# Kernel optimization log

Hardware: AMD Instinct MI355X
Metric: run time of the kernel (lower is better)

Reference implementation:

```python
import jax, jax.numpy as jnp
import numpy as np

N = 10000        # nodes
E = 120000       # edges
IN_W = 6         # in_width
KER_IN = 6       # edge-attr dim
WN = 32          # width_node
WK = 256         # width_kernel
DEPTH = 4


def setup_inputs() -> dict:
    key = jax.random.key(0)
    ks = jax.random.split(key, 16)

    def w(k, shape, fan_in):
        return (jax.random.normal(k, shape, jnp.float32) / np.sqrt(fan_in)).astype(jnp.float32)

    return {
        "x": jax.random.normal(ks[0], (N, IN_W), jnp.float32),
        "edge_index": jax.random.randint(ks[1], (2, E), 0, N, jnp.int64 if jax.config.jax_enable_x64 else jnp.int32),
        "edge_attr": jax.random.uniform(ks[2], (E, KER_IN), jnp.float32),
        # fc1: in_width -> width_node
        "fc1_w": w(ks[3], (IN_W, WN), IN_W), "fc1_b": jnp.zeros((WN,), jnp.float32),
        # DenseNet kernel: ker_in -> WK//2 -> WK -> WN*WN (ReLU between, none after last)
        "k1_w": w(ks[4], (KER_IN, WK // 2), KER_IN), "k1_b": jnp.zeros((WK // 2,), jnp.float32),
        "k2_w": w(ks[5], (WK // 2, WK), WK // 2),    "k2_b": jnp.zeros((WK,), jnp.float32),
        "k3_w": w(ks[6], (WK, WN * WN), WK),         "k3_b": jnp.zeros((WN * WN,), jnp.float32),
        # NNConv root weight + bias
        "root_w": w(ks[7], (WN, WN), WN), "conv_b": jnp.zeros((WN,), jnp.float32),
        # fc2: WN -> 128, fc3: 128 -> 1
        "fc2_w": w(ks[8], (WN, 128), WN), "fc2_b": jnp.zeros((128,), jnp.float32),
        "fc3_w": w(ks[9], (128, 1), 128), "fc3_b": jnp.zeros((1,), jnp.float32),
    }


def reference(x, edge_index, edge_attr,
              fc1_w, fc1_b, k1_w, k1_b, k2_w, k2_b, k3_w, k3_b,
              root_w, conv_b, fc2_w, fc2_b, fc3_w, fc3_b):
    src, dst = edge_index[0], edge_index[1]

    # Edge-conditioned weight matrices via DenseNet kernel MLP (same edge_attr
    # every layer -> identical weights each depth step; compute once).
    h_e = jax.nn.relu(edge_attr @ k1_w + k1_b)
    h_e = jax.nn.relu(h_e @ k2_w + k2_b)
    w_e = (h_e @ k3_w + k3_b).reshape(E, WN, WN)   # [E, in, out]

    # scatter-mean denominator (in-degree, clamped to 1)
    cnt = jax.ops.segment_sum(jnp.ones((E,), jnp.float32), dst, num_segments=N)
    denom = jnp.maximum(cnt, 1.0)[:, None]

    h = x @ fc1_w + fc1_b                          # [N, WN]
    for d in range(DEPTH):
        msg = jnp.einsum('ei,eio->eo', h[src], w_e)          # per-edge matvec
        aggr = jax.ops.segment_sum(msg, dst, num_segments=N) / denom
        h = aggr + h @ root_w + conv_b             # NNConv: aggr + root + bias
        if d != DEPTH - 1:
            h = jax.nn.relu(h)

    h = jax.nn.relu(h @ fc2_w + fc2_b)
    return h @ fc3_w + fc3_b                       # [N, 1]
```

## Files before the change

kernel.cpp:

```cpp
#include <hip/hip_runtime.h>
#include <hip/hip_bf16.h>

#define NN 10000
#define EE 120000
#define E_PAD 120064
#define NT64 1876

#define H1S 136
#define H2S 264

typedef __bf16 bf16_t;
typedef __bf16 bf16x8 __attribute__((ext_vector_type(8)));
typedef float f32x4 __attribute__((ext_vector_type(4)));

static __device__ __forceinline__ int clampi(int v) {
    return v < 0 ? 0 : (v >= NN ? NN - 1 : v);
}

__global__ __launch_bounds__(256) void detect_all(const unsigned short* __restrict__ ea_raw,
                                                  const int* __restrict__ ei,
                                                  int* __restrict__ f32fl,
                                                  int* __restrict__ idxfl) {
    int t = blockIdx.x * 256 + threadIdx.x;
    if (ea_raw[t] & 0x8000) atomicOr(f32fl, 1);
    if (t < 4096 && ei[2 * t + 1] != 0) atomicOr(idxfl, 1);
}

#define N_FLT 16
struct CvtArgs {
    const void* src[N_FLT];
    float* dst;
    int offs[N_FLT];
    int n[N_FLT];
    int tot;
};

__global__ __launch_bounds__(256) void cvt_flat(CvtArgs a, const int* __restrict__ isf32) {
    int i = blockIdx.x * 256 + threadIdx.x;
    if (i >= a.tot) return;
    int t = 0;
#pragma unroll
    for (int k = 1; k < N_FLT; ++k) if (i >= a.offs[k]) t = k;
    int il = i - a.offs[t];
    float v;
    if (*isf32) v = ((const float*)a.src[t])[il];
    else        v = (float)((const bf16_t*)a.src[t])[il];
    if (!isfinite(v)) v = 0.f;
    a.dst[i] = v;
}

__global__ __launch_bounds__(256) void repack_idx(const int* __restrict__ ei,
                                                  const int* __restrict__ flag,
                                                  int* __restrict__ s,
                                                  int* __restrict__ d,
                                                  int* __restrict__ cnti) {
    int e = blockIdx.x * 256 + threadIdx.x;
    if (e >= EE) return;
    int sv, dv;
    if (*flag == 0) {
        sv = clampi(ei[2 * e]);
        dv = clampi(ei[2 * (EE + e)]);
    } else {
        sv = clampi(ei[e]);
        dv = clampi(ei[EE + e]);
    }
    s[e] = sv;
    d[e] = dv;
    atomicAdd(&cnti[dv], 1);
}

__global__ __launch_bounds__(256) void scan_kernel(const int* __restrict__ cnti,
                                                   int* __restrict__ row_off,
                                                   int* __restrict__ pos) {
    __shared__ int part[256];
    const int t = threadIdx.x;
    const int CH = (NN + 255) / 256;
    int s = 0;
    for (int i = 0; i < CH; ++i) {
        int idx = t * CH + i;
        if (idx < NN) s += cnti[idx];
    }
    part[t] = s;
    __syncthreads();
    for (int off = 1; off < 256; off <<= 1) {
        int tmp = (t >= off) ? part[t - off] : 0;
        __syncthreads();
        part[t] += tmp;
        __syncthreads();
    }
    int run = part[t] - s;
    for (int i = 0; i < CH; ++i) {
        int idx = t * CH + i;
        if (idx < NN) {
            row_off[idx] = run;
            pos[idx] = run;
            run += cnti[idx];
        }
    }
    if (t == 255) row_off[NN] = run;
}

__global__ __launch_bounds__(256) void scatter_rank(const int* __restrict__ dst,
                                                    const int* __restrict__ src,
                                                    int* __restrict__ pos,
                                                    int* __restrict__ rank,
                                                    int* __restrict__ src_s) {
    int e = blockIdx.x * 256 + threadIdx.x;
    if (e >= E_PAD) return;
    if (e >= EE) { rank[e] = e; return; }
    int p = atomicAdd(&pos[dst[e]], 1);
    rank[e] = p;
    src_s[p] = src[e];
}

__global__ __launch_bounds__(256) void misc_prep(const float* __restrict__ k2w,
                                                 bf16_t* __restrict__ k2t,
                                                 const float* __restrict__ k3w,
                                                 bf16_t* __restrict__ k3t,
                                                 const float* __restrict__ k3b,
                                                 float* __restrict__ k3bp,
                                                 const float* __restrict__ x,
                                                 const float* __restrict__ fc1w,
                                                 const float* __restrict__ fc1b,
                                                 float* __restrict__ h0) {
    int i = blockIdx.x * 256 + threadIdx.x;
    if (i < 32768) {
        int n = i >> 7, k = i & 127;
        k2t[i] = (bf16_t)k2w[k * 256 + n];
    } else if (i < 294912) {
        int idx = i - 32768;
        int n = idx >> 8, k = idx & 255;
        int c = ((n & 31) << 5) | (n >> 5);
        k3t[idx] = (bf16_t)k3w[k * 1024 + c];
    } else if (i < 295936) {
        int n = i - 294912;
        k3bp[n] = k3b[((n & 31) << 5) | (n >> 5)];
    } else if (i < 615936) {
        int gid = i - 295936;
        int n = gid >> 5, o = gid & 31;
        float acc = fc1b[o];
#pragma unroll
        for (int j = 0; j < 6; ++j) acc += x[n * 6 + j] * fc1w[j * 32 + o];
        h0[gid] = acc;
    }
}

__global__ __launch_bounds__(256, 3) void fused_prep(const float* __restrict__ ea,
                                                     const float* __restrict__ k1w,
                                                     const float* __restrict__ k1b,
                                                     const bf16_t* __restrict__ k2t,
                                                     const float* __restrict__ k2b,
                                                     const bf16_t* __restrict__ k3t,
                                                     const float* __restrict__ k3bp,
                                                     bf16_t* __restrict__ we,
                                                     const int* __restrict__ rank,
                                                     int tile0, int perm) {
    __shared__ bf16_t h1_s[64 * H1S];
    __shared__ bf16_t h2_s[64 * H2S];
    float* ea_s  = (float*)h2_s;
    float* k1w_s = ea_s + 64 * 6;
    float* k1b_s = k1w_s + 768;

    const int t = threadIdx.x;
    const int tile = tile0 + blockIdx.x;
    const int e0 = tile * 64;

    for (int i = t; i < 384; i += 256) {
        int r = i / 6, j = i - r * 6;
        int e = e0 + r;
        ea_s[i] = (e < EE) ? ea[(size_t)e * 6 + j] : 0.f;
    }
    for (int i = t; i < 768; i += 256) k1w_s[i] = k1w[i];
    if (t < 128) k1b_s[t] = k1b[t];
    __syncthreads();

    {
        const int o = t & 127, rh = t >> 7;
        for (int r = rh * 32; r < rh * 32 + 32; ++r) {
            float acc = k1b_s[o];
#pragma unroll
            for (int j = 0; j < 6; ++j) acc += ea_s[r * 6 + j] * k1w_s[j * 128 + o];
            h1_s[r * H1S + o] = (bf16_t)fmaxf(acc, 0.f);
        }
    }
    __syncthreads();

    const int lane = t & 63;
    const int w = t >> 6;
    const int nr16 = lane & 15;
    const int koff = (lane >> 4) * 8;
    const int rbase = (lane >> 4) * 4;

    {
        f32x4 acc[4][4];
#pragma unroll
        for (int i = 0; i < 4; ++i)
#pragma unroll
            for (int j = 0; j < 4; ++j) acc[i][j] = f32x4{0.f, 0.f, 0.f, 0.f};
        bf16x8 bcur[4], bnxt[4];
#pragma unroll
        for (int j = 0; j < 4; ++j)
            bcur[j] = *(const bf16x8*)&k2t[(w * 64 + j * 16 + nr16) * 128 + koff];
#pragma unroll 1
        for (int ks = 0; ks < 4; ++ks) {
            const int k0 = ks * 32;
            if (ks < 3) {
#pragma unroll
                for (int j = 0; j < 4; ++j)
                    bnxt[j] = *(const bf16x8*)&k2t[(w * 64 + j * 16 + nr16) * 128 + k0 + 32 + koff];
            }
            bf16x8 af[4];
#pragma unroll
            for (int i = 0; i < 4; ++i)
                af[i] = *(const bf16x8*)&h1_s[(nr16 + i * 16) * H1S + k0 + koff];
#pragma unroll
            for (int i = 0; i < 4; ++i)
#pragma unroll
                for (int j = 0; j < 4; ++j)
                    acc[i][j] = __builtin_amdgcn_mfma_f32_16x16x32_bf16(af[i], bcur[j], acc[i][j], 0, 0, 0);
#pragma unroll
            for (int j = 0; j < 4; ++j) bcur[j] = bnxt[j];
        }
#pragma unroll
        for (int i = 0; i < 4; ++i) {
#pragma unroll
            for (int j = 0; j < 4; ++j) {
                int col = w * 64 + j * 16 + nr16;
                float bv = k2b[col];
#pragma unroll
                for (int r = 0; r < 4; ++r) {
                    int row = i * 16 + rbase + r;
                    h2_s[row * H2S + col] = (bf16_t)fmaxf(acc[i][j][r] + bv, 0.f);
                }
            }
        }
    }
    __syncthreads();

    int crow[4][4];
#pragma unroll
    for (int i = 0; i < 4; ++i)
#pragma unroll
        for (int r = 0; r < 4; ++r) {
            int lr = i * 16 + rbase + r;
            crow[i][r] = perm ? rank[e0 + lr] : (int)blockIdx.x * 64 + lr;
        }

#pragma unroll 1
    for (int nt = 0; nt < 4; ++nt) {
        const int c0 = nt * 256 + w * 64;
        float bj[4];
#pragma unroll
        for (int j = 0; j < 4; ++j) bj[j] = k3bp[c0 + j * 16 + nr16];
        f32x4 acc[4][4];
#pragma unroll
        for (int i = 0; i < 4; ++i)
#pragma unroll
            for (int j = 0; j < 4; ++j) acc[i][j] = f32x4{0.f, 0.f, 0.f, 0.f};
        bf16x8 bcur[4], bnxt[4];
#pragma unroll
        for (int j = 0; j < 4; ++j)
            bcur[j] = *(const bf16x8*)&k3t[(size_t)(c0 + j * 16 + nr16) * 256 + koff];
#pragma unroll 1
        for (int ks = 0; ks < 8; ++ks) {
            const int k0 = ks * 32;
            if (ks < 7) {
#pragma unroll
                for (int j = 0; j < 4; ++j)
                    bnxt[j] = *(const bf16x8*)&k3t[(size_t)(c0 + j * 16 + nr16) * 256 + k0 + 32 + koff];
            }
            bf16x8 af[4];
#pragma unroll
            for (int i = 0; i < 4; ++i)
                af[i] = *(const bf16x8*)&h2_s[(nr16 + i * 16) * H2S + k0 + koff];
#pragma unroll
            for (int i = 0; i < 4; ++i)
#pragma unroll
                for (int j = 0; j < 4; ++j)
                    acc[i][j] = __builtin_amdgcn_mfma_f32_16x16x32_bf16(af[i], bcur[j], acc[i][j], 0, 0, 0);
#pragma unroll
            for (int j = 0; j < 4; ++j) bcur[j] = bnxt[j];
        }
#pragma unroll
        for (int i = 0; i < 4; ++i) {
#pragma unroll
            for (int r = 0; r < 4; ++r) {
                long cr = crow[i][r];
#pragma unroll
                for (int j = 0; j < 4; ++j) {
                    int col = c0 + j * 16 + nr16;
                    we[cr * 1024 + col] = (bf16_t)(acc[i][j][r] + bj[j]);
                }
            }
        }
    }
}

__global__ __launch_bounds__(256) void gather_stream(const float* __restrict__ h,
                                                     const bf16_t* __restrict__ wt,
                                                     const int* __restrict__ src_s,
                                                     const int* __restrict__ row_off,
                                                     const float* __restrict__ rw,
                                                     const float* __restrict__ cb,
                                                     float* __restrict__ hout,
                                                     int relu, int rev) {
    __shared__ float rws[1024];
    for (int i = threadIdx.x; i < 1024; i += 256) rws[i] = rw[i];
    __syncthreads();
    const int wv = threadIdx.x >> 6, lane = threadIdx.x & 63;
    const int nb = rev ? ((int)gridDim.x - 1 - blockIdx.x) : blockIdx.x;
    const int n = nb * 4 + wv;
    if (n >= NN) return;
    const int o = lane >> 1, half = lane & 1;

    const int b0 = row_off[n], b1 = row_off[n + 1];
    float acc = 0.f;
    if (b0 < b1) {
        int s = src_s[b0];
        const float4* hp = (const float4*)(h + (size_t)s * 32 + half * 16);
        float4 ha = hp[0], hb = hp[1], hcv = hp[2], hd = hp[3];
        const bf16x8* wp = (const bf16x8*)(wt + (size_t)b0 * 1024 + lane * 16);
        bf16x8 w0 = wp[0], w1 = wp[1];
        for (int k = b0; k + 1 < b1; ++k) {
            int s2 = src_s[k + 1];
            const float4* hp2 = (const float4*)(h + (size_t)s2 * 32 + half * 16);
            float4 na = hp2[0], nb2 = hp2[1], nc = hp2[2], nd = hp2[3];
            const bf16x8* wp2 = (const bf16x8*)(wt + (size_t)(k + 1) * 1024 + lane * 16);
            bf16x8 nw0 = wp2[0], nw1 = wp2[1];
            acc += ha.x * (float)w0[0] + ha.y * (float)w0[1]
                 + ha.z * (float)w0[2] + ha.w * (float)w0[3]
                 + hb.x * (float)w0[4] + hb.y * (float)w0[5]
                 + hb.z * (float)w0[6] + hb.w * (float)w0[7]
                 + hcv.x * (float)w1[0] + hcv.y * (float)w1[1]
                 + hcv.z * (float)w1[2] + hcv.w * (float)w1[3]
                 + hd.x * (float)w1[4] + hd.y * (float)w1[5]
                 + hd.z * (float)w1[6] + hd.w * (float)w1[7];
            ha = na; hb = nb2; hcv = nc; hd = nd; w0 = nw0; w1 = nw1;
        }
        acc += ha.x * (float)w0[0] + ha.y * (float)w0[1]
             + ha.z * (float)w0[2] + ha.w * (float)w0[3]
             + hb.x * (float)w0[4] + hb.y * (float)w0[5]
             + hb.z * (float)w0[6] + hb.w * (float)w0[7]
             + hcv.x * (float)w1[0] + hcv.y * (float)w1[1]
             + hcv.z * (float)w1[2] + hcv.w * (float)w1[3]
             + hd.x * (float)w1[4] + hd.y * (float)w1[5]
             + hd.z * (float)w1[6] + hd.w * (float)w1[7];
    }

    float rp = 0.f;
    const float4* hn = (const float4*)(h + (size_t)n * 32 + half * 16);
    float4 a = hn[0], b = hn[1], c = hn[2], dd = hn[3];
    const float* rwb = &rws[half * 16 * 32 + o];
    rp += a.x * rwb[0]   + a.y * rwb[32]  + a.z * rwb[64]  + a.w * rwb[96];
    rp += b.x * rwb[128] + b.y * rwb[160] + b.z * rwb[192] + b.w * rwb[224];
    rp += c.x * rwb[256] + c.y * rwb[288] + c.z * rwb[320] + c.w * rwb[352];
    rp += dd.x * rwb[384] + dd.y * rwb[416] + dd.z * rwb[448] + dd.w * rwb[480];

    acc += __shfl_xor(acc, 1, 64);
    rp  += __shfl_xor(rp, 1, 64);
    if (half == 0) {
        float den = fmaxf((float)(b1 - b0), 1.f);
        float v = acc / den + rp + cb[o];
        if (relu) v = fmaxf(v, 0.f);
        hout[(size_t)n * 32 + o] = v;
    }
}

__global__ __launch_bounds__(256) void edge_scatter(const float* __restrict__ h,
                                                    const bf16_t* __restrict__ wt,
                                                    const int* __restrict__ src,
                                                    const int* __restrict__ dst,
                                                    float* __restrict__ aggr,
                                                    int e0, int e1) {
    int wv = threadIdx.x >> 6, lane = threadIdx.x & 63;
    int e = e0 + blockIdx.x * 4 + wv;
    if (e >= e1) return;
    int s = src[e], d = dst[e];
    int o = lane & 31, ihalf = lane >> 5;
    const float4* hp = (const float4*)(h + (size_t)s * 32 + ihalf * 16);
    float4 ha = hp[0], hb = hp[1], hcv = hp[2], hd = hp[3];
    const bf16x8* wp = (const bf16x8*)(wt + (size_t)(e - e0) * 1024 + o * 32 + ihalf * 16);
    bf16x8 w0 = wp[0], w1 = wp[1];
    float acc = ha.x * (float)w0[0] + ha.y * (float)w0[1]
              + ha.z * (float)w0[2] + ha.w * (float)w0[3]
              + hb.x * (float)w0[4] + hb.y * (float)w0[5]
              + hb.z * (float)w0[6] + hb.w * (float)w0[7]
              + hcv.x * (float)w1[0] + hcv.y * (float)w1[1]
              + hcv.z * (float)w1[2] + hcv.w * (float)w1[3]
              + hd.x * (float)w1[4] + hd.y * (float)w1[5]
              + hd.z * (float)w1[6] + hd.w * (float)w1[7];
    acc += __shfl_xor(acc, 32, 64);
    if (ihalf == 0) atomicAdd(&aggr[(size_t)d * 32 + o], acc);
}

__global__ __launch_bounds__(256) void node_update(const float* __restrict__ hin,
                                                   const float* __restrict__ aggr,
                                                   const int* __restrict__ cnti,
                                                   const float* __restrict__ rw,
                                                   const float* __restrict__ cb,
                                                   float* __restrict__ hout, int relu) {
    __shared__ float rws[32 * 32];
    for (int i = threadIdx.x; i < 1024; i += 256) rws[i] = rw[i];
    __syncthreads();
    int gid = blockIdx.x * 256 + threadIdx.x;
    int n = gid >> 5, o = gid & 31;
    float den = fmaxf((float)cnti[n], 1.f);
    float acc = aggr[gid] / den + cb[o];
    const float* hrow = hin + (size_t)n * 32;
#pragma unroll
    for (int j = 0; j < 32; ++j) acc += hrow[j] * rws[j * 32 + o];
    if (relu) acc = fmaxf(acc, 0.f);
    hout[gid] = acc;
}

__global__ __launch_bounds__(256) void head_kernel(const float* __restrict__ h,
                                                   const float* __restrict__ w2,
                                                   const float* __restrict__ b2,
                                                   const float* __restrict__ w3,
                                                   const float* __restrict__ b3,
                                                   void* __restrict__ out,
                                                   const int* __restrict__ isf32) {
    int wave = threadIdx.x >> 6, lane = threadIdx.x & 63;
    int n = blockIdx.x * 4 + wave;
    if (n >= NN) return;
    const float* hrow = h + (size_t)n * 32;
    float hr[32];
#pragma unroll
    for (int j = 0; j < 32; ++j) hr[j] = hrow[j];
    int o0 = lane * 2, o1 = lane * 2 + 1;
    float v0 = b2[o0], v1 = b2[o1];
#pragma unroll
    for (int j = 0; j < 32; ++j) {
        float hj = hr[j];
        v0 += hj * w2[j * 128 + o0];
        v1 += hj * w2[j * 128 + o1];
    }
    float y = fmaxf(v0, 0.f) * w3[o0] + fmaxf(v1, 0.f) * w3[o1];
#pragma unroll
    for (int m = 1; m < 64; m <<= 1) y += __shfl_xor(y, m, 64);
    if (lane == 0) {
        float r = y + b3[0];
        if (*isf32) ((float*)out)[n] = r;
        else        ((bf16_t*)out)[n] = (bf16_t)r;
    }
}


extern "C" void kernel_launch(void* const* d_in, const int* in_sizes, int n_in,
                              void* d_out, int out_size, void* d_ws, size_t ws_size,
                              hipStream_t stream) {
    const int* ei = (const int*)d_in[1];

    char* ws = (char*)d_ws;
    size_t off = 0;
    auto alignup = [](size_t b) { return (b + 255) & ~(size_t)255; };
    auto alloc = [&](size_t bytes) {
        char* p = ws + off;
        off += alignup(bytes);
        return (void*)p;
    };
    float*  h_a   = (float*)alloc((size_t)NN * 32 * 4);
    float*  h_b   = (float*)alloc((size_t)NN * 32 * 4);
    char*   zbase = ws + off;
    int*    cnti  = (int*)alloc((size_t)NN * 4);
    int*    f32fl = (int*)alloc(256);
    int*    idxfl = (int*)alloc(256);
    size_t  zlen  = (ws + off) - zbase;
    int*    rowo  = (int*)alloc((size_t)(NN + 1) * 4);
    int*    pos   = (int*)alloc((size_t)NN * 4);
    int*    srcb  = (int*)alloc((size_t)EE * 4);
    int*    dstb  = (int*)alloc((size_t)EE * 4);
    int*    rankb = (int*)alloc((size_t)E_PAD * 4);
    int*    src_s = (int*)alloc((size_t)E_PAD * 4);
    bf16_t* k2t   = (bf16_t*)alloc(256 * 128 * 2);
    bf16_t* k3t   = (bf16_t*)alloc(1024 * 256 * 2);
    float*  k3bp  = (float*)alloc(1024 * 4);

    static const int fidx[N_FLT] = {0, 2, 3, 4, 5, 6, 7, 8, 9, 10, 11, 12, 13, 14, 15, 16};
    static const int fn[N_FLT]   = {NN * 6, EE * 6, 192, 32, 768, 128, 32768, 256,
                                    262144, 1024, 1024, 32, 4096, 128, 128, 1};
    int foffs[N_FLT];
    int tot = 0;
    for (int i = 0; i < N_FLT; ++i) { foffs[i] = tot; tot += fn[i]; }
    float* canon = (float*)alloc((size_t)tot * 4);
    const float* c_x    = canon + foffs[0];
    const float* c_ea   = canon + foffs[1];
    const float* c_fc1w = canon + foffs[2];
    const float* c_fc1b = canon + foffs[3];
    const float* c_k1w  = canon + foffs[4];
    const float* c_k1b  = canon + foffs[5];
    const float* c_k2w  = canon + foffs[6];
    const float* c_k2b  = canon + foffs[7];
    const float* c_k3w  = canon + foffs[8];
    const float* c_k3b  = canon + foffs[9];
    const float* c_rw   = canon + foffs[10];
    const float* c_cb   = canon + foffs[11];
    const float* c_fc2w = canon + foffs[12];
    const float* c_fc2b = canon + foffs[13];
    const float* c_fc3w = canon + foffs[14];
    const float* c_fc3b = canon + foffs[15];
    size_t fixed_end = off;

    const size_t sz_we = (size_t)E_PAD * 1024 * 2;
    int mode, T;
    if (ws_size >= fixed_end + sz_we + 1024) { mode = 1; T = NT64; }
    else {
        mode = 0;
        size_t per_tile = (size_t)64 * 1024 * 2;
        size_t extra = alignup((size_t)NN * 32 * 4);
        size_t avail = ws_size > fixed_end + extra + 4096
                     ? ws_size - fixed_end - extra - 4096 : per_tile;
        long t = (long)(avail / per_tile);
        if (t > NT64) t = NT64;
        if (t < 1) t = 1;
        T = (int)t;
    }
    bf16_t* w_e = nullptr;
    float* aggr = nullptr;
    if (mode == 1) {
        w_e = (bf16_t*)alloc(sz_we);
    } else {
        aggr = (float*)alloc((size_t)NN * 32 * 4);
        w_e  = (bf16_t*)alloc((size_t)T * 64 * 1024 * 2);
    }

    hipMemsetAsync(zbase, 0, zlen, stream);

    detect_all<<<32, 256, 0, stream>>>((const unsigned short*)d_in[2], ei, f32fl, idxfl);

    CvtArgs ca;
    for (int i = 0; i < N_FLT; ++i) {
        ca.src[i] = d_in[fidx[i]];
        ca.offs[i] = foffs[i];
        ca.n[i] = fn[i];
    }
    ca.dst = canon;
    ca.tot = tot;
    cvt_flat<<<(tot + 255) / 256, 256, 0, stream>>>(ca, f32fl);

    repack_idx<<<(EE + 255) / 256, 256, 0, stream>>>(ei, idxfl, srcb, dstb, cnti);
    scan_kernel<<<1, 256, 0, stream>>>(cnti, rowo, pos);
    scatter_rank<<<(E_PAD + 255) / 256, 256, 0, stream>>>(dstb, srcb, pos, rankb, src_s);

    misc_prep<<<(615936 + 255) / 256, 256, 0, stream>>>(c_k2w, k2t, c_k3w, k3t,
                                                        c_k3b, k3bp, c_x, c_fc1w,
                                                        c_fc1b, h_a);

    float* hc = h_a;
    float* hn = h_b;
    if (mode == 1) {
        fused_prep<<<NT64, 256, 0, stream>>>(c_ea, c_k1w, c_k1b, k2t, c_k2b,
                                             k3t, k3bp, w_e, rankb, 0, 1);
        for (int d = 0; d < 4; ++d) {
            gather_stream<<<(NN + 3) / 4, 256, 0, stream>>>(hc, w_e, src_s, rowo,
                                                            c_rw, c_cb, hn,
                                                            (d < 3) ? 1 : 0, d & 1);
            float* tmp = hc; hc = hn; hn = tmp;
        }
    } else {
        for (int d = 0; d < 4; ++d) {
            hipMemsetAsync(aggr, 0, (size_t)NN * 32 * 4, stream);
            for (int t0 = 0; t0 < NT64; t0 += T) {
                int tl = (t0 + T <= NT64) ? T : (NT64 - t0);
                fused_prep<<<tl, 256, 0, stream>>>(c_ea, c_k1w, c_k1b, k2t, c_k2b,
                                                   k3t, k3bp, w_e, rankb, t0, 0);
                int e0 = t0 * 64;
                int e1 = e0 + tl * 64; if (e1 > EE) e1 = EE;
                if (e1 > e0)
                    edge_scatter<<<(e1 - e0 + 3) / 4, 256, 0, stream>>>(hc, w_e, srcb, dstb,
                                                                        aggr, e0, e1);
            }
            node_update<<<NN * 32 / 256, 256, 0, stream>>>(hc, aggr, cnti, c_rw, c_cb, hn,
                                                           (d < 3) ? 1 : 0);
            float* tmp = hc; hc = hn; hn = tmp;
        }
    }

    head_kernel<<<(NN + 3) / 4, 256, 0, stream>>>(hc, c_fc2w, c_fc2b, c_fc3w, c_fc3b,
                                                  d_out, f32fl);
}
```

Measured before the change: 492.7 us.

## Halve edge tile to 32 rows and vectorize w_e stores via column permutation

```diff
diff --git a/kernel.cpp b/kernel.cpp
--- a/kernel.cpp
+++ b/kernel.cpp
@@ -4,13 +4,14 @@
 #define NN 10000
 #define EE 120000
 #define E_PAD 120064
-#define NT64 1876
+#define NT32 3752
 
 #define H1S 136
 #define H2S 264
 
 typedef __bf16 bf16_t;
 typedef __bf16 bf16x8 __attribute__((ext_vector_type(8)));
+typedef __bf16 bf16x4 __attribute__((ext_vector_type(4)));
 typedef float f32x4 __attribute__((ext_vector_type(4)));
 
 static __device__ __forceinline__ int clampi(int v) {
@@ -113,6 +114,12 @@
     src_s[p] = src[e];
 }
 
+static __device__ __forceinline__ int slot_logical(int n) {
+    int p = n & 63;
+    int q = ((p & 15) << 2) | (p >> 4);
+    return (n & ~63) | q;
+}
+
 __global__ __launch_bounds__(256) void misc_prep(const float* __restrict__ k2w,
                                                  bf16_t* __restrict__ k2t,
                                                  const float* __restrict__ k3w,
@@ -126,15 +133,18 @@
     int i = blockIdx.x * 256 + threadIdx.x;
     if (i < 32768) {
         int n = i >> 7, k = i & 127;
-        k2t[i] = (bf16_t)k2w[k * 256 + n];
+        int m = slot_logical(n);
+        k2t[i] = (bf16_t)k2w[k * 256 + m];
     } else if (i < 294912) {
         int idx = i - 32768;
         int n = idx >> 8, k = idx & 255;
-        int c = ((n & 31) << 5) | (n >> 5);
+        int m = slot_logical(n);
+        int c = ((m & 31) << 5) | (m >> 5);
         k3t[idx] = (bf16_t)k3w[k * 1024 + c];
     } else if (i < 295936) {
         int n = i - 294912;
-        k3bp[n] = k3b[((n & 31) << 5) | (n >> 5)];
+        int m = slot_logical(n);
+        k3bp[n] = k3b[((m & 31) << 5) | (m >> 5)];
     } else if (i < 615936) {
         int gid = i - 295936;
         int n = gid >> 5, o = gid & 31;
@@ -145,7 +155,7 @@
     }
 }
 
-__global__ __launch_bounds__(256, 3) void fused_prep(const float* __restrict__ ea,
+__global__ __launch_bounds__(256, 6) void fused_prep(const float* __restrict__ ea,
                                                      const float* __restrict__ k1w,
                                                      const float* __restrict__ k1b,
                                                      const bf16_t* __restrict__ k2t,
@@ -155,20 +165,19 @@
                                                      bf16_t* __restrict__ we,
                                                      const int* __restrict__ rank,
                                                      int tile0, int perm) {
-    __shared__ bf16_t h1_s[64 * H1S];
-    __shared__ bf16_t h2_s[64 * H2S];
+    __shared__ bf16_t h1_s[32 * H1S];
+    __shared__ bf16_t h2_s[32 * H2S];
     float* ea_s  = (float*)h2_s;
-    float* k1w_s = ea_s + 64 * 6;
+    float* k1w_s = ea_s + 192;
     float* k1b_s = k1w_s + 768;
 
     const int t = threadIdx.x;
-    const int tile = tile0 + blockIdx.x;
-    const int e0 = tile * 64;
-
-    for (int i = t; i < 384; i += 256) {
-        int r = i / 6, j = i - r * 6;
+    const int e0 = (tile0 + blockIdx.x) * 32;
+
+    if (t < 192) {
+        int r = t / 6, j = t - r * 6;
         int e = e0 + r;
-        ea_s[i] = (e < EE) ? ea[(size_t)e * 6 + j] : 0.f;
+        ea_s[t] = (e < EE) ? ea[(size_t)e * 6 + j] : 0.f;
     }
     for (int i = t; i < 768; i += 256) k1w_s[i] = k1w[i];
     if (t < 128) k1b_s[t] = k1b[t];
@@ -176,7 +185,7 @@
 
     {
         const int o = t & 127, rh = t >> 7;
-        for (int r = rh * 32; r < rh * 32 + 32; ++r) {
+        for (int r = rh * 16; r < rh * 16 + 16; ++r) {
             float acc = k1b_s[o];
 #pragma unroll
             for (int j = 0; j < 6; ++j) acc += ea_s[r * 6 + j] * k1w_s[j * 128 + o];
@@ -192,9 +201,9 @@
     const int rbase = (lane >> 4) * 4;
 
     {
-        f32x4 acc[4][4];
-#pragma unroll
-        for (int i = 0; i < 4; ++i)
+        f32x4 acc[2][4];
+#pragma unroll
+        for (int i = 0; i < 2; ++i)
 #pragma unroll
             for (int j = 0; j < 4; ++j) acc[i][j] = f32x4{0.f, 0.f, 0.f, 0.f};
         bf16x8 bcur[4], bnxt[4];
@@ -209,41 +218,42 @@
                 for (int j = 0; j < 4; ++j)
                     bnxt[j] = *(const bf16x8*)&k2t[(w * 64 + j * 16 + nr16) * 128 + k0 + 32 + koff];
             }
-            bf16x8 af[4];
-#pragma unroll
-            for (int i = 0; i < 4; ++i)
+            bf16x8 af[2];
+#pragma unroll
+            for (int i = 0; i < 2; ++i)
                 af[i] = *(const bf16x8*)&h1_s[(nr16 + i * 16) * H1S + k0 + koff];
 #pragma unroll
-            for (int i = 0; i < 4; ++i)
+            for (int i = 0; i < 2; ++i)
 #pragma unroll
                 for (int j = 0; j < 4; ++j)
                     acc[i][j] = __builtin_amdgcn_mfma_f32_16x16x32_bf16(af[i], bcur[j], acc[i][j], 0, 0, 0);
 #pragma unroll
             for (int j = 0; j < 4; ++j) bcur[j] = bnxt[j];
         }
-#pragma unroll
-        for (int i = 0; i < 4; ++i) {
-#pragma unroll
-            for (int j = 0; j < 4; ++j) {
-                int col = w * 64 + j * 16 + nr16;
-                float bv = k2b[col];
-#pragma unroll
-                for (int r = 0; r < 4; ++r) {
-                    int row = i * 16 + rbase + r;
-                    h2_s[row * H2S + col] = (bf16_t)fmaxf(acc[i][j][r] + bv, 0.f);
-                }
+        float bj[4];
+#pragma unroll
+        for (int j = 0; j < 4; ++j) bj[j] = k2b[w * 64 + nr16 * 4 + j];
+#pragma unroll
+        for (int i = 0; i < 2; ++i) {
+#pragma unroll
+            for (int r = 0; r < 4; ++r) {
+                int row = i * 16 + rbase + r;
+                bf16x4 v;
+#pragma unroll
+                for (int j = 0; j < 4; ++j) v[j] = (bf16_t)fmaxf(acc[i][j][r] + bj[j], 0.f);
+                *(bf16x4*)&h2_s[row * H2S + w * 64 + nr16 * 4] = v;
             }
         }
     }
     __syncthreads();
 
-    int crow[4][4];
-#pragma unroll
-    for (int i = 0; i < 4; ++i)
+    int crow[2][4];
+#pragma unroll
+    for (int i = 0; i < 2; ++i)
 #pragma unroll
         for (int r = 0; r < 4; ++r) {
             int lr = i * 16 + rbase + r;
-            crow[i][r] = perm ? rank[e0 + lr] : (int)blockIdx.x * 64 + lr;
+            crow[i][r] = perm ? rank[e0 + lr] : (int)blockIdx.x * 32 + lr;
         }
 
 #pragma unroll 1
@@ -252,9 +262,9 @@
         float bj[4];
 #pragma unroll
         for (int j = 0; j < 4; ++j) bj[j] = k3bp[c0 + j * 16 + nr16];
-        f32x4 acc[4][4];
-#pragma unroll
-        for (int i = 0; i < 4; ++i)
+        f32x4 acc[2][4];
+#pragma unroll
+        for (int i = 0; i < 2; ++i)
 #pragma unroll
             for (int j = 0; j < 4; ++j) acc[i][j] = f32x4{0.f, 0.f, 0.f, 0.f};
         bf16x8 bcur[4], bnxt[4];
@@ -269,12 +279,12 @@
                 for (int j = 0; j < 4; ++j)
                     bnxt[j] = *(const bf16x8*)&k3t[(size_t)(c0 + j * 16 + nr16) * 256 + k0 + 32 + koff];
             }
-            bf16x8 af[4];
-#pragma unroll
-            for (int i = 0; i < 4; ++i)
+            bf16x8 af[2];
+#pragma unroll
+            for (int i = 0; i < 2; ++i)
                 af[i] = *(const bf16x8*)&h2_s[(nr16 + i * 16) * H2S + k0 + koff];
 #pragma unroll
-            for (int i = 0; i < 4; ++i)
+            for (int i = 0; i < 2; ++i)
 #pragma unroll
                 for (int j = 0; j < 4; ++j)
                     acc[i][j] = __builtin_amdgcn_mfma_f32_16x16x32_bf16(af[i], bcur[j], acc[i][j], 0, 0, 0);
@@ -282,15 +292,14 @@
             for (int j = 0; j < 4; ++j) bcur[j] = bnxt[j];
         }
 #pragma unroll
-        for (int i = 0; i < 4; ++i) {
+        for (int i = 0; i < 2; ++i) {
 #pragma unroll
             for (int r = 0; r < 4; ++r) {
                 long cr = crow[i][r];
-#pragma unroll
-                for (int j = 0; j < 4; ++j) {
-                    int col = c0 + j * 16 + nr16;
-                    we[cr * 1024 + col] = (bf16_t)(acc[i][j][r] + bj[j]);
-                }
+                bf16x4 v;
+#pragma unroll
+                for (int j = 0; j < 4; ++j) v[j] = (bf16_t)(acc[i][j][r] + bj[j]);
+                *(bf16x4*)&we[cr * 1024 + c0 + nr16 * 4] = v;
             }
         }
     }
@@ -503,15 +512,15 @@
 
     const size_t sz_we = (size_t)E_PAD * 1024 * 2;
     int mode, T;
-    if (ws_size >= fixed_end + sz_we + 1024) { mode = 1; T = NT64; }
+    if (ws_size >= fixed_end + sz_we + 1024) { mode = 1; T = NT32; }
     else {
         mode = 0;
-        size_t per_tile = (size_t)64 * 1024 * 2;
+        size_t per_tile = (size_t)32 * 1024 * 2;
         size_t extra = alignup((size_t)NN * 32 * 4);
         size_t avail = ws_size > fixed_end + extra + 4096
                      ? ws_size - fixed_end - extra - 4096 : per_tile;
         long t = (long)(avail / per_tile);
-        if (t > NT64) t = NT64;
+        if (t > NT32) t = NT32;
         if (t < 1) t = 1;
         T = (int)t;
     }
@@ -521,7 +530,7 @@
         w_e = (bf16_t*)alloc(sz_we);
     } else {
         aggr = (float*)alloc((size_t)NN * 32 * 4);
-        w_e  = (bf16_t*)alloc((size_t)T * 64 * 1024 * 2);
+        w_e  = (bf16_t*)alloc((size_t)T * 32 * 1024 * 2);
     }
 
     hipMemsetAsync(zbase, 0, zlen, stream);
@@ -549,7 +558,7 @@
     float* hc = h_a;
     float* hn = h_b;
     if (mode == 1) {
-        fused_prep<<<NT64, 256, 0, stream>>>(c_ea, c_k1w, c_k1b, k2t, c_k2b,
+        fused_prep<<<NT32, 256, 0, stream>>>(c_ea, c_k1w, c_k1b, k2t, c_k2b,
                                              k3t, k3bp, w_e, rankb, 0, 1);
         for (int d = 0; d < 4; ++d) {
             gather_stream<<<(NN + 3) / 4, 256, 0, stream>>>(hc, w_e, src_s, rowo,
@@ -560,12 +569,12 @@
     } else {
         for (int d = 0; d < 4; ++d) {
             hipMemsetAsync(aggr, 0, (size_t)NN * 32 * 4, stream);
-            for (int t0 = 0; t0 < NT64; t0 += T) {
-                int tl = (t0 + T <= NT64) ? T : (NT64 - t0);
+            for (int t0 = 0; t0 < NT32; t0 += T) {
+                int tl = (t0 + T <= NT32) ? T : (NT32 - t0);
                 fused_prep<<<tl, 256, 0, stream>>>(c_ea, c_k1w, c_k1b, k2t, c_k2b,
                                                    k3t, k3bp, w_e, rankb, t0, 0);
-                int e0 = t0 * 64;
-                int e1 = e0 + tl * 64; if (e1 > EE) e1 = EE;
+                int e0 = t0 * 32;
+                int e1 = e0 + tl * 32; if (e1 > EE) e1 = EE;
                 if (e1 > e0)
                     edge_scatter<<<(e1 - e0 + 3) / 4, 256, 0, stream>>>(hc, w_e, srcb, dstb,
                                                                         aggr, e0, e1);
```

New measurement: 646.8 us. 31.3% more time.

## Permute weight column order for vectorized bf16x4 stores and triple-buffer k3 loads

Applied to the files above, without the earlier changes.

```diff
diff --git a/kernel.cpp b/kernel.cpp
--- a/kernel.cpp
+++ b/kernel.cpp
@@ -11,6 +11,7 @@
 
 typedef __bf16 bf16_t;
 typedef __bf16 bf16x8 __attribute__((ext_vector_type(8)));
+typedef __bf16 bf16x4 __attribute__((ext_vector_type(4)));
 typedef float f32x4 __attribute__((ext_vector_type(4)));
 
 static __device__ __forceinline__ int clampi(int v) {
@@ -113,6 +114,12 @@
     src_s[p] = src[e];
 }
 
+static __device__ __forceinline__ int slot_logical(int n) {
+    int p = n & 63;
+    int q = ((p & 15) << 2) | (p >> 4);
+    return (n & ~63) | q;
+}
+
 __global__ __launch_bounds__(256) void misc_prep(const float* __restrict__ k2w,
                                                  bf16_t* __restrict__ k2t,
                                                  const float* __restrict__ k3w,
@@ -126,15 +133,18 @@
     int i = blockIdx.x * 256 + threadIdx.x;
     if (i < 32768) {
         int n = i >> 7, k = i & 127;
-        k2t[i] = (bf16_t)k2w[k * 256 + n];
+        int m = slot_logical(n);
+        k2t[i] = (bf16_t)k2w[k * 256 + m];
     } else if (i < 294912) {
         int idx = i - 32768;
         int n = idx >> 8, k = idx & 255;
-        int c = ((n & 31) << 5) | (n >> 5);
+        int m = slot_logical(n);
+        int c = ((m & 31) << 5) | (m >> 5);
         k3t[idx] = (bf16_t)k3w[k * 1024 + c];
     } else if (i < 295936) {
         int n = i - 294912;
-        k3bp[n] = k3b[((n & 31) << 5) | (n >> 5)];
+        int m = slot_logical(n);
+        k3bp[n] = k3b[((m & 31) << 5) | (m >> 5)];
     } else if (i < 615936) {
         int gid = i - 295936;
         int n = gid >> 5, o = gid & 31;
@@ -158,12 +168,11 @@
     __shared__ bf16_t h1_s[64 * H1S];
     __shared__ bf16_t h2_s[64 * H2S];
     float* ea_s  = (float*)h2_s;
-    float* k1w_s = ea_s + 64 * 6;
+    float* k1w_s = ea_s + 384;
     float* k1b_s = k1w_s + 768;
 
     const int t = threadIdx.x;
-    const int tile = tile0 + blockIdx.x;
-    const int e0 = tile * 64;
+    const int e0 = (tile0 + blockIdx.x) * 64;
 
     for (int i = t; i < 384; i += 256) {
         int r = i / 6, j = i - r * 6;
@@ -221,17 +230,18 @@
 #pragma unroll
             for (int j = 0; j < 4; ++j) bcur[j] = bnxt[j];
         }
+        float bj[4];
+#pragma unroll
+        for (int j = 0; j < 4; ++j) bj[j] = k2b[w * 64 + nr16 * 4 + j];
 #pragma unroll
         for (int i = 0; i < 4; ++i) {
 #pragma unroll
-            for (int j = 0; j < 4; ++j) {
-                int col = w * 64 + j * 16 + nr16;
-                float bv = k2b[col];
-#pragma unroll
-                for (int r = 0; r < 4; ++r) {
-                    int row = i * 16 + rbase + r;
-                    h2_s[row * H2S + col] = (bf16_t)fmaxf(acc[i][j][r] + bv, 0.f);
-                }
+            for (int r = 0; r < 4; ++r) {
+                int row = i * 16 + rbase + r;
+                bf16x4 v;
+#pragma unroll
+                for (int j = 0; j < 4; ++j) v[j] = (bf16_t)fmaxf(acc[i][j][r] + bj[j], 0.f);
+                *(bf16x4*)&h2_s[row * H2S + w * 64 + nr16 * 4] = v;
             }
         }
     }
@@ -249,6 +259,10 @@
 #pragma unroll 1
     for (int nt = 0; nt < 4; ++nt) {
         const int c0 = nt * 256 + w * 64;
+        const bf16_t* bp[4];
+#pragma unroll
+        for (int j = 0; j < 4; ++j)
+            bp[j] = &k3t[(size_t)(c0 + j * 16 + nr16) * 256 + koff];
         float bj[4];
 #pragma unroll
         for (int j = 0; j < 4; ++j) bj[j] = k3bp[c0 + j * 16 + nr16];
@@ -257,17 +271,18 @@
         for (int i = 0; i < 4; ++i)
 #pragma unroll
             for (int j = 0; j < 4; ++j) acc[i][j] = f32x4{0.f, 0.f, 0.f, 0.f};
-        bf16x8 bcur[4], bnxt[4];
-#pragma unroll
-        for (int j = 0; j < 4; ++j)
-            bcur[j] = *(const bf16x8*)&k3t[(size_t)(c0 + j * 16 + nr16) * 256 + koff];
-#pragma unroll 1
+        bf16x8 bb[3][4];
+#pragma unroll
+        for (int j = 0; j < 4; ++j) bb[0][j] = *(const bf16x8*)(bp[j]);
+#pragma unroll
+        for (int j = 0; j < 4; ++j) bb[1][j] = *(const bf16x8*)(bp[j] + 32);
+#pragma unroll
         for (int ks = 0; ks < 8; ++ks) {
             const int k0 = ks * 32;
-            if (ks < 7) {
+            if (ks < 6) {
 #pragma unroll
                 for (int j = 0; j < 4; ++j)
-                    bnxt[j] = *(const bf16x8*)&k3t[(size_t)(c0 + j * 16 + nr16) * 256 + k0 + 32 + koff];
+                    bb[(ks + 2) % 3][j] = *(const bf16x8*)(bp[j] + k0 + 64);
             }
             bf16x8 af[4];
 #pragma unroll
@@ -277,20 +292,17 @@
             for (int i = 0; i < 4; ++i)
 #pragma unroll
                 for (int j = 0; j < 4; ++j)
-                    acc[i][j] = __builtin_amdgcn_mfma_f32_16x16x32_bf16(af[i], bcur[j], acc[i][j], 0, 0, 0);
-#pragma unroll
-            for (int j = 0; j < 4; ++j) bcur[j] = bnxt[j];
+                    acc[i][j] = __builtin_amdgcn_mfma_f32_16x16x32_bf16(af[i], bb[ks % 3][j], acc[i][j], 0, 0, 0);
         }
 #pragma unroll
         for (int i = 0; i < 4; ++i) {
 #pragma unroll
             for (int r = 0; r < 4; ++r) {
                 long cr = crow[i][r];
-#pragma unroll
-                for (int j = 0; j < 4; ++j) {
-                    int col = c0 + j * 16 + nr16;
-                    we[cr * 1024 + col] = (bf16_t)(acc[i][j][r] + bj[j]);
-                }
+                bf16x4 v;
+#pragma unroll
+                for (int j = 0; j < 4; ++j) v[j] = (bf16_t)(acc[i][j][r] + bj[j]);
+                *(bf16x4*)&we[cr * 1024 + c0 + nr16 * 4] = v;
             }
         }
     }
```

After: 634.5 us. 28.8% more time.
